# Kernel optimization log

Hardware: AMD Instinct MI355X
Metric: run time of the kernel (lower is better)

The kernel has to match this reference:

```python
import jax, jax.numpy as jnp
import numpy as np
import math

D_MODEL = 1024
NHEAD = 16
D_K = D_MODEL // NHEAD
B, S = 2, 2048


def setup_inputs() -> dict:
    key = jax.random.key(0)
    ks = jax.random.split(key, 9)
    x = jax.random.normal(ks[0], (B, S, D_MODEL), dtype=jnp.float32)
    # causal mask, broadcastable to (B, nhead, S, S); 0 entries are masked out
    mask = jnp.tril(jnp.ones((S, S), dtype=jnp.int32))[None, None, :, :]
    scale = 1.0 / math.sqrt(D_MODEL)
    def lin(kw, kb):
        W = jax.random.uniform(kw, (D_MODEL, D_MODEL), dtype=jnp.float32, minval=-scale, maxval=scale)
        b = jax.random.uniform(kb, (D_MODEL,), dtype=jnp.float32, minval=-scale, maxval=scale)
        return W, b
    Wq, bq = lin(ks[1], ks[2])
    Wk, bk = lin(ks[3], ks[4])
    Wv, bv = lin(ks[5], ks[6])
    Wo, bo = lin(ks[7], ks[8])
    return {"x": x, "mask": mask, "Wq": Wq, "bq": bq, "Wk": Wk, "bk": bk,
            "Wv": Wv, "bv": bv, "Wo": Wo, "bo": bo}


def reference(x, mask, Wq, bq, Wk, bk, Wv, bv, Wo, bo):
    b, s, _ = x.shape
    def heads(W, bias):
        # (b, s, d_model) @ (d_model, d_model) -> (b, nhead, s, d_k)
        return (x @ W.T + bias).reshape(b, s, NHEAD, D_K).transpose(0, 2, 1, 3)
    Q, K, V = heads(Wq, bq), heads(Wk, bk), heads(Wv, bv)
    scores = jnp.einsum('bhqd,bhkd->bhqk', Q, K) / math.sqrt(D_K)
    scores = jnp.where(mask == 0, jnp.float32(-1e9), scores)
    attn = jax.nn.softmax(scores, axis=-1)  # dropout is identity in eval mode
    out = jnp.einsum('bhqk,bhkd->bhqd', attn, V)
    out = out.transpose(0, 2, 1, 3).reshape(b, s, D_MODEL)
    return out @ Wo.T + bo
```

## Files before the change

kernel.cpp:

```cpp
#include <hip/hip_runtime.h>
#include <hip/hip_bf16.h>

#define DMODEL 1024
#define NH     16
#define DKH    64
#define BSZ    2
#define SEQ    2048
#define MROWS  (BSZ*SEQ)
#define WELEM  (DMODEL*DMODEL)

typedef __attribute__((ext_vector_type(8))) short short8;
typedef __attribute__((ext_vector_type(4))) float f32x4;

__device__ __forceinline__ ushort f2bf(float f) {
    return __bfloat16_as_ushort(__float2bfloat16(f));
}
__device__ __forceinline__ unsigned pk2(float lo, float hi) {
    return (unsigned)f2bf(lo) | ((unsigned)f2bf(hi) << 16);
}
__device__ __forceinline__ void load_lds16(const ushort* g, ushort* l) {
    __builtin_amdgcn_global_load_lds(
        (const __attribute__((address_space(1))) unsigned int*)g,
        (__attribute__((address_space(3))) unsigned int*)l, 16, 0, 0);
}

__global__ __launch_bounds__(256)
void cvt_all(const float* __restrict__ x,
             const float* __restrict__ W0, const float* __restrict__ W1,
             const float* __restrict__ W2, const float* __restrict__ W3,
             ushort* __restrict__ xbf, ushort* __restrict__ Wcat,
             ushort* __restrict__ Wo)
{
    const int blk = blockIdx.x;
    const float* src;
    ushort* dst;
    int base;
    if (blk < 2048)      { src = x;  dst = xbf;             base = blk * 2048; }
    else if (blk < 2560) { src = W0; dst = Wcat;            base = (blk - 2048) * 2048; }
    else if (blk < 3072) { src = W1; dst = Wcat + WELEM;    base = (blk - 2560) * 2048; }
    else if (blk < 3584) { src = W2; dst = Wcat + 2*WELEM;  base = (blk - 3072) * 2048; }
    else                 { src = W3; dst = Wo;              base = (blk - 3584) * 2048; }
    const size_t off = (size_t)base + threadIdx.x * 8;
    const float4 f0 = *(const float4*)(src + off);
    const float4 f1 = *(const float4*)(src + off + 4);
    uint4 o;
    o.x = pk2(f0.x, f0.y); o.y = pk2(f0.z, f0.w);
    o.z = pk2(f1.x, f1.y); o.w = pk2(f1.z, f1.w);
    *(uint4*)(dst + off) = o;
}

__global__ __launch_bounds__(256)
void gemm_qkv(const ushort* __restrict__ xbf, const ushort* __restrict__ Wcat,
              const float* __restrict__ bq, const float* __restrict__ bk,
              const float* __restrict__ bv,
              ushort* __restrict__ Qh, ushort* __restrict__ Kh,
              ushort* __restrict__ VT)
{
    __shared__ ushort Ash[128][32];
    __shared__ ushort Bsh[128][32];

    const int t    = threadIdx.x;
    const int m0   = blockIdx.y * 128, n0 = blockIdx.x * 128;
    const int wave = t >> 6;
    const int lane = t & 63;
    const int wr   = (wave >> 1) * 64;
    const int wc   = (wave & 1) * 64;
    const int quad = lane >> 4;
    const int r16  = lane & 15;

    const int row0 = wave * 16 + (lane >> 2);
    const int row1 = 64 + wave * 16 + (lane >> 2);
    const int ch   = (lane & 3) * 8;

    f32x4 acc[4][4];
    #pragma unroll
    for (int i = 0; i < 4; ++i)
        #pragma unroll
        for (int j = 0; j < 4; ++j)
            acc[i][j] = (f32x4){0.f, 0.f, 0.f, 0.f};

    for (int k0 = 0; k0 < DMODEL; k0 += 32) {
        load_lds16(xbf  + (size_t)(m0 + row0) * DMODEL + k0 + ch, &Ash[wave * 16][0]);
        load_lds16(xbf  + (size_t)(m0 + row1) * DMODEL + k0 + ch, &Ash[64 + wave * 16][0]);
        load_lds16(Wcat + (size_t)(n0 + row0) * DMODEL + k0 + ch, &Bsh[wave * 16][0]);
        load_lds16(Wcat + (size_t)(n0 + row1) * DMODEL + k0 + ch, &Bsh[64 + wave * 16][0]);
        __syncthreads();

        short8 af[4], bf[4];
        #pragma unroll
        for (int i = 0; i < 4; ++i) af[i] = *(const short8*)&Ash[wr + i * 16 + r16][quad * 8];
        #pragma unroll
        for (int j = 0; j < 4; ++j) bf[j] = *(const short8*)&Bsh[wc + j * 16 + r16][quad * 8];

        #pragma unroll
        for (int i = 0; i < 4; ++i)
            #pragma unroll
            for (int j = 0; j < 4; ++j)
                acc[i][j] = __builtin_amdgcn_mfma_f32_16x16x32_bf16(af[i], bf[j], acc[i][j], 0, 0, 0);
        __syncthreads();
    }

    const int region = n0 >> 10;
    const float* bp  = (region == 0) ? bq : (region == 1) ? bk : bv;
    ushort* outQK    = (region == 0) ? Qh : Kh;
    const float osc  = (region == 0) ? 0.18033688f : 1.0f;
    const int nbase  = n0 & 1023;

    #pragma unroll
    for (int i = 0; i < 4; ++i) {
        #pragma unroll
        for (int j = 0; j < 4; ++j) {
            #pragma unroll
            for (int reg = 0; reg < 4; ++reg) {
                const int m  = m0 + wr + i * 16 + quad * 4 + reg;
                const int n  = nbase + wc + j * 16 + r16;
                const float v = (acc[i][j][reg] + bp[n]) * osc;
                const int b = m >> 11, s = m & (SEQ - 1);
                const int h = n >> 6,  dk = n & 63;
                if (region < 2) {
                    outQK[((size_t)(b * NH + h) * SEQ + s) * DKH + dk] = f2bf(v);
                } else {
                    VT[(((size_t)(b * NH + h)) * DKH + dk) * SEQ + s] = f2bf(v);
                }
            }
        }
    }
}

__global__ __launch_bounds__(256)
void gemm_out(const ushort* __restrict__ O, const ushort* __restrict__ Wo,
              const float* __restrict__ bo, float* __restrict__ out)
{
    __shared__ ushort Ash[128][32];
    __shared__ ushort Bsh[64][32];

    const int t    = threadIdx.x;
    const int m0   = blockIdx.y * 128, n0 = blockIdx.x * 64;
    const int wave = t >> 6;
    const int lane = t & 63;
    const int wr   = (wave >> 1) * 64;
    const int wc   = (wave & 1) * 32;
    const int quad = lane >> 4;
    const int r16  = lane & 15;

    const int row0 = wave * 16 + (lane >> 2);
    const int row1 = 64 + wave * 16 + (lane >> 2);
    const int ch   = (lane & 3) * 8;

    f32x4 acc[4][2];
    #pragma unroll
    for (int i = 0; i < 4; ++i)
        #pragma unroll
        for (int j = 0; j < 2; ++j)
            acc[i][j] = (f32x4){0.f, 0.f, 0.f, 0.f};

    for (int k0 = 0; k0 < DMODEL; k0 += 32) {
        const int ma0 = m0 + row0, ma1 = m0 + row1;
        load_lds16(O + ((size_t)(ma0 >> 11) * NH + (k0 >> 6)) * (SEQ * DKH)
                     + (size_t)(ma0 & (SEQ - 1)) * DKH + (k0 & 63) + ch,
                   &Ash[wave * 16][0]);
        load_lds16(O + ((size_t)(ma1 >> 11) * NH + (k0 >> 6)) * (SEQ * DKH)
                     + (size_t)(ma1 & (SEQ - 1)) * DKH + (k0 & 63) + ch,
                   &Ash[64 + wave * 16][0]);
        load_lds16(Wo + (size_t)(n0 + row0) * DMODEL + k0 + ch, &Bsh[wave * 16][0]);
        __syncthreads();

        short8 af[4], bf[2];
        #pragma unroll
        for (int i = 0; i < 4; ++i) af[i] = *(const short8*)&Ash[wr + i * 16 + r16][quad * 8];
        #pragma unroll
        for (int j = 0; j < 2; ++j) bf[j] = *(const short8*)&Bsh[wc + j * 16 + r16][quad * 8];

        #pragma unroll
        for (int i = 0; i < 4; ++i)
            #pragma unroll
            for (int j = 0; j < 2; ++j)
                acc[i][j] = __builtin_amdgcn_mfma_f32_16x16x32_bf16(af[i], bf[j], acc[i][j], 0, 0, 0);
        __syncthreads();
    }

    #pragma unroll
    for (int i = 0; i < 4; ++i) {
        #pragma unroll
        for (int j = 0; j < 2; ++j) {
            #pragma unroll
            for (int reg = 0; reg < 4; ++reg) {
                const int m = m0 + wr + i * 16 + quad * 4 + reg;
                const int n = n0 + wc + j * 16 + r16;
                out[(size_t)m * DMODEL + n] = acc[i][j][reg] + bo[n];
            }
        }
    }
}

__global__ __launch_bounds__(256)
void gemm_mfma(const void* __restrict__ A, const void* __restrict__ W,
               const float* __restrict__ bias, void* __restrict__ out,
               int amode, int bmode, int outmode, float oscale)
{
    __shared__ ushort Ash[128][40];
    __shared__ ushort Bsh[128][40];

    const int t    = threadIdx.x;
    const int m0   = blockIdx.y * 128, n0 = blockIdx.x * 128;
    const int srow = t >> 1;
    const int shal = (t & 1) * 16;

    const int wave = t >> 6;
    const int lane = t & 63;
    const int wr   = (wave >> 1) * 64;
    const int wc   = (wave & 1) * 64;
    const int quad = lane >> 4;
    const int r16  = lane & 15;

    f32x4 acc[4][4];
    #pragma unroll
    for (int i = 0; i < 4; ++i)
        #pragma unroll
        for (int j = 0; j < 4; ++j)
            acc[i][j] = (f32x4){0.f, 0.f, 0.f, 0.f};

    for (int k0 = 0; k0 < DMODEL; k0 += 32) {
        uint4 a01, a23, b01, b23;
        if (amode == 0) {
            const float* ap = (const float*)A + (size_t)(m0 + srow) * DMODEL + k0 + shal;
            const float4 f0 = *(const float4*)(ap);
            const float4 f1 = *(const float4*)(ap + 4);
            const float4 f2 = *(const float4*)(ap + 8);
            const float4 f3 = *(const float4*)(ap + 12);
            a01 = (uint4){pk2(f0.x,f0.y), pk2(f0.z,f0.w), pk2(f1.x,f1.y), pk2(f1.z,f1.w)};
            a23 = (uint4){pk2(f2.x,f2.y), pk2(f2.z,f2.w), pk2(f3.x,f3.y), pk2(f3.z,f3.w)};
        } else if (amode == 1) {
            const int m = m0 + srow;
            const ushort* ap = (const ushort*)A
                + ((size_t)(m >> 11) * NH + (k0 >> 6)) * (SEQ * DKH)
                + (size_t)(m & (SEQ - 1)) * DKH + (k0 & 63) + shal;
            a01 = *(const uint4*)(ap);
            a23 = *(const uint4*)(ap + 8);
        } else {
            const ushort* ap = (const ushort*)A + (size_t)(m0 + srow) * DMODEL + k0 + shal;
            a01 = *(const uint4*)(ap);
            a23 = *(const uint4*)(ap + 8);
        }
        if (bmode == 0) {
            const float* wp = (const float*)W + (size_t)(n0 + srow) * DMODEL + k0 + shal;
            const float4 w0 = *(const float4*)(wp);
            const float4 w1 = *(const float4*)(wp + 4);
            const float4 w2 = *(const float4*)(wp + 8);
            const float4 w3 = *(const float4*)(wp + 12);
            b01 = (uint4){pk2(w0.x,w0.y), pk2(w0.z,w0.w), pk2(w1.x,w1.y), pk2(w1.z,w1.w)};
            b23 = (uint4){pk2(w2.x,w2.y), pk2(w2.z,w2.w), pk2(w3.x,w3.y), pk2(w3.z,w3.w)};
        } else {
            const ushort* wp = (const ushort*)W + (size_t)(n0 + srow) * DMODEL + k0 + shal;
            b01 = *(const uint4*)(wp);
            b23 = *(const uint4*)(wp + 8);
        }

        *(uint4*)&Ash[srow][shal]     = a01;
        *(uint4*)&Ash[srow][shal + 8] = a23;
        *(uint4*)&Bsh[srow][shal]     = b01;
        *(uint4*)&Bsh[srow][shal + 8] = b23;
        __syncthreads();

        short8 af[4], bf[4];
        #pragma unroll
        for (int i = 0; i < 4; ++i) af[i] = *(const short8*)&Ash[wr + i * 16 + r16][quad * 8];
        #pragma unroll
        for (int j = 0; j < 4; ++j) bf[j] = *(const short8*)&Bsh[wc + j * 16 + r16][quad * 8];

        #pragma unroll
        for (int i = 0; i < 4; ++i)
            #pragma unroll
            for (int j = 0; j < 4; ++j)
                acc[i][j] = __builtin_amdgcn_mfma_f32_16x16x32_bf16(af[i], bf[j], acc[i][j], 0, 0, 0);
        __syncthreads();
    }

    #pragma unroll
    for (int i = 0; i < 4; ++i) {
        #pragma unroll
        for (int j = 0; j < 4; ++j) {
            #pragma unroll
            for (int reg = 0; reg < 4; ++reg) {
                const int m = m0 + wr + i * 16 + quad * 4 + reg;
                const int n = n0 + wc + j * 16 + r16;
                const float v = (acc[i][j][reg] + bias[n]) * oscale;
                if (outmode == 0) {
                    ((float*)out)[(size_t)m * DMODEL + n] = v;
                } else if (outmode == 1) {
                    ((ushort*)out)[((size_t)(m >> 11) * NH + (n >> 6)) * (SEQ * DKH)
                                   + (size_t)(m & (SEQ - 1)) * DKH + (n & 63)] = f2bf(v);
                } else {
                    ((ushort*)out)[(((size_t)(m >> 11) * NH + (n >> 6)) * DKH + (n & 63)) * SEQ
                                   + (m & (SEQ - 1))] = f2bf(v);
                }
            }
        }
    }
}

__global__ __launch_bounds__(256)
void attn_flash(ushort* __restrict__ Qh,
                const ushort* __restrict__ Kh,
                const ushort* __restrict__ VT)
{
    __shared__ ushort Kl[128][72];
    __shared__ ushort Vl[64][136];
    __shared__ ushort Pl[4][16][136];

    const int t256 = threadIdx.x;
    const int wave = t256 >> 6;
    const int lane = t256 & 63;
    const int quad = lane >> 4;
    const int r16  = lane & 15;

    const int slot = blockIdx.x & 7;
    const int bh   = slot * 4 + ((blockIdx.x >> 3) & 3);
    const int qt   = blockIdx.x >> 5;
    const int q0   = qt * 64;

    ushort*       Qbase = Qh + (size_t)bh * SEQ * DKH;
    const ushort* Kbase = Kh + (size_t)bh * SEQ * DKH;
    const ushort* Vbase = VT + (size_t)bh * DKH * SEQ;

    short8 qf[2];
    {
        const ushort* qrow = Qbase + (size_t)(q0 + wave * 16 + r16) * DKH;
        qf[0] = *(const short8*)(qrow + quad * 8);
        qf[1] = *(const short8*)(qrow + 32 + quad * 8);
    }

    f32x4 oacc[4];
    #pragma unroll
    for (int i = 0; i < 4; ++i) oacc[i] = (f32x4){0.f, 0.f, 0.f, 0.f};
    float lsum = 0.f;

    const int T    = (qt >> 1) + 1;
    const int off  = (qt & 1) * 64;
    const int qrel = off + wave * 16 + r16;

    const int krow = t256 >> 1, kc = (t256 & 1) * 32;
    const int vrow = t256 >> 2, vc = (t256 & 3) * 32;
    const ushort* kg0 = Kbase + (size_t)krow * DKH + kc;
    const ushort* vg0 = Vbase + (size_t)vrow * SEQ + vc;

    uint4 kr0, kr1, kr2, kr3, vr0, vr1, vr2, vr3;
    {
        kr0 = *(const uint4*)(kg0);
        kr1 = *(const uint4*)(kg0 + 8);
        kr2 = *(const uint4*)(kg0 + 16);
        kr3 = *(const uint4*)(kg0 + 24);
        vr0 = *(const uint4*)(vg0);
        vr1 = *(const uint4*)(vg0 + 8);
        vr2 = *(const uint4*)(vg0 + 16);
        vr3 = *(const uint4*)(vg0 + 24);
    }

    for (int t = 0; t < T; ++t) {
        *(uint4*)&Kl[krow][kc]      = kr0;
        *(uint4*)&Kl[krow][kc + 8]  = kr1;
        *(uint4*)&Kl[krow][kc + 16] = kr2;
        *(uint4*)&Kl[krow][kc + 24] = kr3;
        *(uint4*)&Vl[vrow][vc]      = vr0;
        *(uint4*)&Vl[vrow][vc + 8]  = vr1;
        *(uint4*)&Vl[vrow][vc + 16] = vr2;
        *(uint4*)&Vl[vrow][vc + 24] = vr3;
        __syncthreads();

        if (t + 1 < T) {
            const ushort* kg = kg0 + (size_t)(t + 1) * 128 * DKH;
            kr0 = *(const uint4*)(kg);
            kr1 = *(const uint4*)(kg + 8);
            kr2 = *(const uint4*)(kg + 16);
            kr3 = *(const uint4*)(kg + 24);
            const ushort* vg = vg0 + (size_t)(t + 1) * 128;
            vr0 = *(const uint4*)(vg);
            vr1 = *(const uint4*)(vg + 8);
            vr2 = *(const uint4*)(vg + 16);
            vr3 = *(const uint4*)(vg + 24);
        }

        f32x4 sacc[8];
        __builtin_amdgcn_s_setprio(1);
        #pragma unroll
        for (int nt = 0; nt < 8; ++nt) {
            short8 b0 = *(const short8*)&Kl[nt * 16 + r16][quad * 8];
            short8 b1 = *(const short8*)&Kl[nt * 16 + r16][32 + quad * 8];
            sacc[nt] = (f32x4){0.f, 0.f, 0.f, 0.f};
            sacc[nt] = __builtin_amdgcn_mfma_f32_16x16x32_bf16(b0, qf[0], sacc[nt], 0, 0, 0);
            sacc[nt] = __builtin_amdgcn_mfma_f32_16x16x32_bf16(b1, qf[1], sacc[nt], 0, 0, 0);
        }
        __builtin_amdgcn_s_setprio(0);

        const bool diag = (t == T - 1);
        #pragma unroll
        for (int nt = 0; nt < 8; ++nt) {
            float pv[4];
            #pragma unroll
            for (int reg = 0; reg < 4; ++reg) {
                float e = __builtin_amdgcn_exp2f(sacc[nt][reg]);
                if (diag && (nt * 16 + quad * 4 + reg) > qrel) e = 0.f;
                pv[reg] = e;
                lsum += e;
            }
            uint2 w;
            w.x = pk2(pv[0], pv[1]);
            w.y = pk2(pv[2], pv[3]);
            *(uint2*)&Pl[wave][r16][nt * 16 + quad * 4] = w;
        }

        __builtin_amdgcn_s_setprio(1);
        #pragma unroll
        for (int c = 0; c < 4; ++c) {
            short8 af = *(const short8*)&Pl[wave][r16][c * 32 + quad * 8];
            #pragma unroll
            for (int ct = 0; ct < 4; ++ct) {
                short8 bf = *(const short8*)&Vl[ct * 16 + r16][c * 32 + quad * 8];
                oacc[ct] = __builtin_amdgcn_mfma_f32_16x16x32_bf16(af, bf, oacc[ct], 0, 0, 0);
            }
        }
        __builtin_amdgcn_s_setprio(0);
        __syncthreads();
    }

    lsum += __shfl_xor(lsum, 16, 64);
    lsum += __shfl_xor(lsum, 32, 64);

    #pragma unroll
    for (int reg = 0; reg < 4; ++reg) {
        const float inv = 1.f / __shfl(lsum, quad * 4 + reg, 64);
        const int q = q0 + wave * 16 + quad * 4 + reg;
        ushort* orow = Qbase + (size_t)q * DKH;
        #pragma unroll
        for (int ct = 0; ct < 4; ++ct)
            orow[ct * 16 + r16] = f2bf(oacc[ct][reg] * inv);
    }
}

extern "C" void kernel_launch(void* const* d_in, const int* in_sizes, int n_in,
                              void* d_out, int out_size, void* d_ws, size_t ws_size,
                              hipStream_t stream)
{
    const float* x  = (const float*)d_in[0];
    const float* Wf[4] = {(const float*)d_in[2], (const float*)d_in[4],
                          (const float*)d_in[6], (const float*)d_in[8]};
    const float* Bf[4] = {(const float*)d_in[3], (const float*)d_in[5],
                          (const float*)d_in[7], (const float*)d_in[9]};

    const size_t HSZ = (size_t)MROWS * DMODEL;
    ushort* Qh = (ushort*)d_ws;
    ushort* Kh = (ushort*)d_out;
    ushort* VT = (ushort*)d_out + HSZ;

    const dim3 blk(256);

    if (ws_size >= 24u * 1024 * 1024) {
        ushort* Wcat = Qh + HSZ;
        ushort* Wo   = Wcat + 3 * (size_t)WELEM;
        ushort* xbf  = Wo + WELEM;

        cvt_all<<<dim3(4096), blk, 0, stream>>>(x, Wf[0], Wf[1], Wf[2], Wf[3],
                                                xbf, Wcat, Wo);

        gemm_qkv<<<dim3(3 * DMODEL / 128, MROWS / 128), blk, 0, stream>>>(
            xbf, Wcat, Bf[0], Bf[1], Bf[2], Qh, Kh, VT);

        attn_flash<<<dim3(BSZ * NH * 32), blk, 0, stream>>>(Qh, Kh, VT);

        gemm_out<<<dim3(DMODEL / 64, MROWS / 128), blk, 0, stream>>>(
            Qh, Wo, Bf[3], (float*)d_out);
    } else {
        const dim3 gg(DMODEL / 128, MROWS / 128);
        gemm_mfma<<<gg, blk, 0, stream>>>(x, Wf[0], Bf[0], Qh, 0, 0, 1, 0.18033688f);
        gemm_mfma<<<gg, blk, 0, stream>>>(x, Wf[1], Bf[1], Kh, 0, 0, 1, 1.0f);
        gemm_mfma<<<gg, blk, 0, stream>>>(x, Wf[2], Bf[2], VT, 0, 0, 2, 1.0f);
        attn_flash<<<dim3(BSZ * NH * 32), blk, 0, stream>>>(Qh, Kh, VT);
        gemm_mfma<<<gg, blk, 0, stream>>>(Qh, Wf[3], Bf[3], d_out, 1, 0, 0, 1.0f);
    }
}
```

Baseline: 200.1 us.

## Enlarge attention Q tile to 128 rows with 8 waves and peel masked diagonal

The flash attention kernel now uses 512-thread blocks covering 128 query rows, so each K/V tile loaded into LDS is shared by twice as many waves and K/V traffic is halved. The causal diagonal tile is peeled out of the main loop. Each wave there skips score and PV MFMAs for fully masked columns, and the main loop loses the per-element mask check. Blocks are ordered heaviest-first to balance the triangular workload. The risks are fewer blocks (512 instead of 1024) and higher register and LDS pressure per block.

```diff
diff --git a/kernel.cpp b/kernel.cpp
--- a/kernel.cpp
+++ b/kernel.cpp
@@ -299,25 +299,25 @@
     }
 }
 
-__global__ __launch_bounds__(256)
+__global__ __launch_bounds__(512, 4)
 void attn_flash(ushort* __restrict__ Qh,
                 const ushort* __restrict__ Kh,
                 const ushort* __restrict__ VT)
 {
     __shared__ ushort Kl[128][72];
     __shared__ ushort Vl[64][136];
-    __shared__ ushort Pl[4][16][136];
-
-    const int t256 = threadIdx.x;
-    const int wave = t256 >> 6;
-    const int lane = t256 & 63;
+    __shared__ ushort Pl[8][16][136];
+
+    const int t512 = threadIdx.x;
+    const int wave = t512 >> 6;
+    const int lane = t512 & 63;
     const int quad = lane >> 4;
     const int r16  = lane & 15;
 
     const int slot = blockIdx.x & 7;
     const int bh   = slot * 4 + ((blockIdx.x >> 3) & 3);
-    const int qt   = blockIdx.x >> 5;
-    const int q0   = qt * 64;
+    const int qt   = 15 - (blockIdx.x >> 5);
+    const int q0   = qt * 128;
 
     ushort*       Qbase = Qh + (size_t)bh * SEQ * DKH;
     const ushort* Kbase = Kh + (size_t)bh * SEQ * DKH;
@@ -333,51 +333,36 @@
     f32x4 oacc[4];
     #pragma unroll
     for (int i = 0; i < 4; ++i) oacc[i] = (f32x4){0.f, 0.f, 0.f, 0.f};
-    float lsum = 0.f;
-
-    const int T    = (qt >> 1) + 1;
-    const int off  = (qt & 1) * 64;
-    const int qrel = off + wave * 16 + r16;
-
-    const int krow = t256 >> 1, kc = (t256 & 1) * 32;
-    const int vrow = t256 >> 2, vc = (t256 & 3) * 32;
+    f32x4 lsum4 = (f32x4){0.f, 0.f, 0.f, 0.f};
+
+    const int T    = qt + 1;
+    const int qrel = wave * 16 + r16;
+
+    const int krow = t512 >> 2, kc = (t512 & 3) * 16;
+    const int vrow = t512 >> 3, vc = (t512 & 7) * 16;
     const ushort* kg0 = Kbase + (size_t)krow * DKH + kc;
     const ushort* vg0 = Vbase + (size_t)vrow * SEQ + vc;
 
-    uint4 kr0, kr1, kr2, kr3, vr0, vr1, vr2, vr3;
-    {
-        kr0 = *(const uint4*)(kg0);
-        kr1 = *(const uint4*)(kg0 + 8);
-        kr2 = *(const uint4*)(kg0 + 16);
-        kr3 = *(const uint4*)(kg0 + 24);
-        vr0 = *(const uint4*)(vg0);
-        vr1 = *(const uint4*)(vg0 + 8);
-        vr2 = *(const uint4*)(vg0 + 16);
-        vr3 = *(const uint4*)(vg0 + 24);
-    }
-
-    for (int t = 0; t < T; ++t) {
-        *(uint4*)&Kl[krow][kc]      = kr0;
-        *(uint4*)&Kl[krow][kc + 8]  = kr1;
-        *(uint4*)&Kl[krow][kc + 16] = kr2;
-        *(uint4*)&Kl[krow][kc + 24] = kr3;
-        *(uint4*)&Vl[vrow][vc]      = vr0;
-        *(uint4*)&Vl[vrow][vc + 8]  = vr1;
-        *(uint4*)&Vl[vrow][vc + 16] = vr2;
-        *(uint4*)&Vl[vrow][vc + 24] = vr3;
-        __syncthreads();
-
-        if (t + 1 < T) {
+    uint4 kr0, kr1, vr0, vr1;
+    kr0 = *(const uint4*)(kg0);
+    kr1 = *(const uint4*)(kg0 + 8);
+    vr0 = *(const uint4*)(vg0);
+    vr1 = *(const uint4*)(vg0 + 8);
+
+    for (int t = 0; t < T - 1; ++t) {
+        *(uint4*)&Kl[krow][kc]     = kr0;
+        *(uint4*)&Kl[krow][kc + 8] = kr1;
+        *(uint4*)&Vl[vrow][vc]     = vr0;
+        *(uint4*)&Vl[vrow][vc + 8] = vr1;
+        __syncthreads();
+
+        {
             const ushort* kg = kg0 + (size_t)(t + 1) * 128 * DKH;
             kr0 = *(const uint4*)(kg);
             kr1 = *(const uint4*)(kg + 8);
-            kr2 = *(const uint4*)(kg + 16);
-            kr3 = *(const uint4*)(kg + 24);
             const ushort* vg = vg0 + (size_t)(t + 1) * 128;
             vr0 = *(const uint4*)(vg);
             vr1 = *(const uint4*)(vg + 8);
-            vr2 = *(const uint4*)(vg + 16);
-            vr3 = *(const uint4*)(vg + 24);
         }
 
         f32x4 sacc[8];
@@ -392,20 +377,16 @@
         }
         __builtin_amdgcn_s_setprio(0);
 
-        const bool diag = (t == T - 1);
         #pragma unroll
         for (int nt = 0; nt < 8; ++nt) {
-            float pv[4];
-            #pragma unroll
-            for (int reg = 0; reg < 4; ++reg) {
-                float e = __builtin_amdgcn_exp2f(sacc[nt][reg]);
-                if (diag && (nt * 16 + quad * 4 + reg) > qrel) e = 0.f;
-                pv[reg] = e;
-                lsum += e;
-            }
+            const float e0 = __builtin_amdgcn_exp2f(sacc[nt][0]);
+            const float e1 = __builtin_amdgcn_exp2f(sacc[nt][1]);
+            const float e2 = __builtin_amdgcn_exp2f(sacc[nt][2]);
+            const float e3 = __builtin_amdgcn_exp2f(sacc[nt][3]);
+            lsum4 += (f32x4){e0, e1, e2, e3};
             uint2 w;
-            w.x = pk2(pv[0], pv[1]);
-            w.y = pk2(pv[2], pv[3]);
+            w.x = pk2(e0, e1);
+            w.y = pk2(e2, e3);
             *(uint2*)&Pl[wave][r16][nt * 16 + quad * 4] = w;
         }
 
@@ -423,6 +404,64 @@
         __syncthreads();
     }
 
+    {
+        *(uint4*)&Kl[krow][kc]     = kr0;
+        *(uint4*)&Kl[krow][kc + 8] = kr1;
+        *(uint4*)&Vl[vrow][vc]     = vr0;
+        *(uint4*)&Vl[vrow][vc + 8] = vr1;
+        __syncthreads();
+
+        const int ntmax = wave | 1;
+        const int cmax  = wave >> 1;
+
+        f32x4 sacc[8];
+        __builtin_amdgcn_s_setprio(1);
+        #pragma unroll
+        for (int nt = 0; nt < 8; ++nt) {
+            if (nt <= ntmax) {
+                short8 b0 = *(const short8*)&Kl[nt * 16 + r16][quad * 8];
+                short8 b1 = *(const short8*)&Kl[nt * 16 + r16][32 + quad * 8];
+                sacc[nt] = (f32x4){0.f, 0.f, 0.f, 0.f};
+                sacc[nt] = __builtin_amdgcn_mfma_f32_16x16x32_bf16(b0, qf[0], sacc[nt], 0, 0, 0);
+                sacc[nt] = __builtin_amdgcn_mfma_f32_16x16x32_bf16(b1, qf[1], sacc[nt], 0, 0, 0);
+            }
+        }
+        __builtin_amdgcn_s_setprio(0);
+
+        #pragma unroll
+        for (int nt = 0; nt < 8; ++nt) {
+            if (nt <= ntmax) {
+                float pv[4];
+                #pragma unroll
+                for (int reg = 0; reg < 4; ++reg) {
+                    float e = __builtin_amdgcn_exp2f(sacc[nt][reg]);
+                    if ((nt * 16 + quad * 4 + reg) > qrel) e = 0.f;
+                    pv[reg] = e;
+                }
+                lsum4 += (f32x4){pv[0], pv[1], pv[2], pv[3]};
+                uint2 w;
+                w.x = pk2(pv[0], pv[1]);
+                w.y = pk2(pv[2], pv[3]);
+                *(uint2*)&Pl[wave][r16][nt * 16 + quad * 4] = w;
+            }
+        }
+
+        __builtin_amdgcn_s_setprio(1);
+        #pragma unroll
+        for (int c = 0; c < 4; ++c) {
+            if (c <= cmax) {
+                short8 af = *(const short8*)&Pl[wave][r16][c * 32 + quad * 8];
+                #pragma unroll
+                for (int ct = 0; ct < 4; ++ct) {
+                    short8 bf = *(const short8*)&Vl[ct * 16 + r16][c * 32 + quad * 8];
+                    oacc[ct] = __builtin_amdgcn_mfma_f32_16x16x32_bf16(af, bf, oacc[ct], 0, 0, 0);
+                }
+            }
+        }
+        __builtin_amdgcn_s_setprio(0);
+    }
+
+    float lsum = (lsum4[0] + lsum4[1]) + (lsum4[2] + lsum4[3]);
     lsum += __shfl_xor(lsum, 16, 64);
     lsum += __shfl_xor(lsum, 32, 64);
 
@@ -465,7 +504,7 @@
         gemm_qkv<<<dim3(3 * DMODEL / 128, MROWS / 128), blk, 0, stream>>>(
             xbf, Wcat, Bf[0], Bf[1], Bf[2], Qh, Kh, VT);
 
-        attn_flash<<<dim3(BSZ * NH * 32), blk, 0, stream>>>(Qh, Kh, VT);
+        attn_flash<<<dim3(BSZ * NH * 16), dim3(512), 0, stream>>>(Qh, Kh, VT);
 
         gemm_out<<<dim3(DMODEL / 64, MROWS / 128), blk, 0, stream>>>(
             Qh, Wo, Bf[3], (float*)d_out);
@@ -474,7 +513,7 @@
         gemm_mfma<<<gg, blk, 0, stream>>>(x, Wf[0], Bf[0], Qh, 0, 0, 1, 0.18033688f);
         gemm_mfma<<<gg, blk, 0, stream>>>(x, Wf[1], Bf[1], Kh, 0, 0, 1, 1.0f);
         gemm_mfma<<<gg, blk, 0, stream>>>(x, Wf[2], Bf[2], VT, 0, 0, 2, 1.0f);
-        attn_flash<<<dim3(BSZ * NH * 32), blk, 0, stream>>>(Qh, Kh, VT);
+        attn_flash<<<dim3(BSZ * NH * 16), dim3(512), 0, stream>>>(Qh, Kh, VT);
         gemm_mfma<<<gg, blk, 0, stream>>>(Qh, Wf[3], Bf[3], d_out, 1, 0, 0, 1.0f);
     }
 }
```

After: 200.3 us. Within noise of the previous version (+0.1%).
